# Performance work log

Hardware: AMD Instinct MI355X
Metric: run time of the kernel (lower is better)

The kernel has to match this reference:

```python
import jax, jax.numpy as jnp
import numpy as np

B, F, H, W, C = 1, 16, 32, 32, 128


def setup_inputs() -> dict:
    key = jax.random.key(0)
    ks = jax.random.split(key, 6)
    w = lambda k: jax.random.normal(k, (C, C), jnp.float32) * 0.02
    return {
        "x": jax.random.normal(ks[0], (B, F, H, W, C), jnp.float32),
        "gamma": jnp.ones((C,), jnp.float32),
        "wq": w(ks[1]), "bq": jnp.zeros((C,), jnp.float32),
        "wk": w(ks[2]), "bk": jnp.zeros((C,), jnp.float32),
        "wv": w(ks[3]), "bv": jnp.zeros((C,), jnp.float32),
        "wo": w(ks[4]), "bo": jnp.zeros((C,), jnp.float32),
    }


def reference(x, gamma, wq, bq, wk, bk, wv, bv, wo, bo):
    b, f, h, w_, c = x.shape
    s, n_hw = f * h * w_, h * w_
    identity = x

    # RMSNorm variant: L2-normalize over channels, rescale by sqrt(C) * gamma
    xn = x / (jnp.linalg.norm(x, axis=-1, keepdims=True) + 1e-8)
    xn = xn * (c ** 0.5) * gamma

    # 1x1x1 convs == pointwise linear projections; flatten to tokens [b, s, c]
    xn = xn.reshape(b, s, c)
    q = xn @ wq + bq
    k = xn @ wk + bk
    v = xn @ wv + bv

    # frame-causal block mask: query at frame i attends to all keys in frames <= i
    frame = jnp.arange(s) // n_hw                      # [s]
    allowed = frame[:, None] >= frame[None, :]          # [s, s] bool

    scale = 1.0 / jnp.sqrt(c)
    scores = jnp.einsum('bqc,bkc->bqk', q, k) * scale   # [b, s, s]
    scores = jnp.where(allowed, scores, -jnp.inf)
    attn = jax.nn.softmax(scores, axis=-1)
    out = jnp.einsum('bqk,bkc->bqc', attn, v)           # [b, s, c]

    out = out @ wo + bo
    return out.reshape(b, f, h, w_, c) + identity
```

## Files before the change

kernel.cpp:

```cpp
#include <hip/hip_runtime.h>
#include <hip/hip_bf16.h>

typedef __bf16 bf16x8 __attribute__((ext_vector_type(8)));
typedef float f32x4 __attribute__((ext_vector_type(4)));
typedef unsigned short u16;
typedef unsigned int u32;
typedef u16 ushort8 __attribute__((ext_vector_type(8)));

#define S_TOK 16384
#define C_DIM 128
#define L2E 1.4426950408889634f
#define QK_SCALE 0.08838834764831845f
#define SQRTC 11.313708498984761f

#define NBLK 512
#define TPB 34

#define WT_OFF   0u
#define BIAS_OFF 131072u
#define XN_OFF   147456u
#define O_OFF    XN_OFF
#define Q_OFF    (XN_OFF + 4194304u)
#define K_OFF    (Q_OFF + 4194304u)
#define VF_OFF   (K_OFF + 4194304u)
#define PART_OFF (VF_OFF + 4194304u)
#define ML_OFF   (PART_OFF + 20971520u)

__device__ __forceinline__ int in_is_bf16(const void* gamma) {
  return ((const u16*)gamma)[0] == 0x3F80;
}
__device__ __forceinline__ float ldf(const void* p, int i, int bf) {
  if (bf) { u32 b = ((const u16*)p)[i]; return __uint_as_float(b << 16); }
  return ((const float*)p)[i];
}
__device__ __forceinline__ float b2f(u16 b) { return __uint_as_float((u32)b << 16); }
__device__ __forceinline__ u16 f2b(float f) {
  return __builtin_bit_cast(u16, (__bf16)f);
}
__device__ __forceinline__ void gld16(const void* g, void* l) {
  __builtin_amdgcn_global_load_lds((const __attribute__((address_space(1))) u32*)g,
                                   (__attribute__((address_space(3))) u32*)l, 16, 0, 0);
}
__device__ __forceinline__ int qb_of(int t) {
  int F = 0;
  while (64 * (F + 1) * (F + 2) <= t) F++;
  int span = 16 * (F + 1);
  return 8 * F + (t - 64 * F * (F + 1)) / span;
}
__device__ __forceinline__ int start_of(int qq) {
  int Fq = qq >> 3, iq = qq & 7;
  return 16 * (Fq + 1) * (4 * Fq + iq);
}

__global__ void __launch_bounds__(256) prep_norm_kernel(const void* x, const void* gamma,
    const void* wq, const void* bq, const void* wk, const void* bk,
    const void* wv, const void* bv, const void* wo, const void* bo, char* ws) {
  int bf = in_is_bf16(gamma);
  if (blockIdx.x >= 2048) {
    int bb = blockIdx.x - 2048;
    if (bb < 256) {
      int gid = bb * 256 + threadIdx.x;
      int m = gid >> 14; int rem = gid & 16383;
      int k = rem >> 7; int n = rem & 127;
      const void* W = (m == 0) ? wq : (m == 1) ? wk : (m == 2) ? wv : wo;
      float v = ldf(W, rem, bf);
      if (m == 0) v *= QK_SCALE;
      *(u16*)(ws + WT_OFF + (u32)m * 32768u + (u32)n * 256u + (((u32)k * 2u) ^ (u32)((n & 7) << 4))) = f2b(v);
    } else {
      int idx = (bb - 256) * 256 + threadIdx.x;
      if (idx < 512) {
        int m = idx >> 7; int c = idx & 127;
        const void* B = (m == 0) ? bq : (m == 1) ? bk : (m == 2) ? bv : bo;
        float v = ldf(B, c, bf);
        if (m == 0) v *= QK_SCALE;
        ((float*)(ws + BIAS_OFF))[idx] = v;
      }
    }
    return;
  }
  int t = blockIdx.x * 256 + threadIdx.x;
  int tok = t >> 5; int sub = t & 31;
  int base = tok * 128 + sub * 4;
  float f[4];
  if (bf) {
    ushort4 v = ((const ushort4*)x)[base >> 2];
    f[0] = __uint_as_float((u32)v.x << 16); f[1] = __uint_as_float((u32)v.y << 16);
    f[2] = __uint_as_float((u32)v.z << 16); f[3] = __uint_as_float((u32)v.w << 16);
  } else {
    float4 v = ((const float4*)x)[base >> 2];
    f[0] = v.x; f[1] = v.y; f[2] = v.z; f[3] = v.w;
  }
  float ss = f[0]*f[0] + f[1]*f[1] + f[2]*f[2] + f[3]*f[3];
  #pragma unroll
  for (int m = 1; m < 32; m <<= 1) ss += __shfl_xor(ss, m);
  float fac = SQRTC / (sqrtf(ss) + 1e-8f);
  u16 o[4];
  #pragma unroll
  for (int j = 0; j < 4; j++) { float g = ldf(gamma, sub * 4 + j, bf); o[j] = f2b(f[j] * fac * g); }
  *(ushort4*)(ws + XN_OFF + (u32)tok * 256u + (((u32)sub * 8u) ^ (u32)((tok & 7) << 4))) =
      make_ushort4(o[0], o[1], o[2], o[3]);
}

__global__ void __launch_bounds__(256) qkv_kernel(char* ws) {
  __shared__ char lds[65536];
  int tid = threadIdx.x; int wid = tid >> 6; int lane = tid & 63;
  int blk = blockIdx.x & 127;
  int m = blockIdx.x >> 7;
  #pragma unroll
  for (int i = 0; i < 8; i++) {
    u32 seg = (u32)(i * 4 + wid) * 1024u;
    gld16(ws + XN_OFF + (u32)blk * 32768u + seg + (u32)lane * 16u, lds + seg);
    gld16(ws + WT_OFF + (u32)m * 32768u + seg + (u32)lane * 16u, lds + 32768 + seg);
  }
  __syncthreads();
  const float* bias = (const float*)(ws + BIAS_OFF);
  int rb = wid * 32;
  f32x4 acc[2][8];
  #pragma unroll
  for (int a = 0; a < 2; a++)
    #pragma unroll
    for (int b = 0; b < 8; b++) acc[a][b] = (f32x4){0.f, 0.f, 0.f, 0.f};
  #pragma unroll
  for (int kt = 0; kt < 4; kt++) {
    bf16x8 afr[2];
    #pragma unroll
    for (int mt = 0; mt < 2; mt++) {
      int row = rb + mt * 16 + (lane & 15);
      afr[mt] = *(const bf16x8*)(lds + row * 256 + ((kt * 64 + ((lane >> 4) * 16)) ^ ((row & 7) << 4)));
    }
    #pragma unroll
    for (int nt = 0; nt < 8; nt++) {
      int nr = nt * 16 + (lane & 15);
      bf16x8 bfr = *(const bf16x8*)(lds + 32768 + nr * 256 + ((kt * 64 + ((lane >> 4) * 16)) ^ ((nr & 7) << 4)));
      #pragma unroll
      for (int mt = 0; mt < 2; mt++)
        acc[mt][nt] = __builtin_amdgcn_mfma_f32_16x16x32_bf16(afr[mt], bfr, acc[mt][nt], 0, 0, 0);
    }
  }
  #pragma unroll
  for (int mt = 0; mt < 2; mt++)
    #pragma unroll
    for (int nt = 0; nt < 8; nt++) {
      int tok0 = blk * 128 + rb + mt * 16 + (lane >> 4) * 4;
      int c = (lane & 15) + nt * 16;
      float bv_ = bias[m * 128 + c];
      if (m == 0) {
        #pragma unroll
        for (int r = 0; r < 4; r++)
          *(u16*)(ws + Q_OFF + ((u32)(tok0 + r) * 128u + (u32)c) * 2u) = f2b(acc[mt][nt][r] + bv_);
      } else if (m == 1) {
        int ktc = c >> 5, gc = (c >> 3) & 3, jc = c & 7;
        int tile = tok0 >> 6, ntk = (tok0 >> 4) & 3, qv0 = tok0 & 15;
        char* bp = ws + K_OFF + (u32)tile * 16384u + (u32)(ktc * 4 + ntk) * 1024u + (u32)(16 * gc) * 16u + (u32)jc * 2u;
        #pragma unroll
        for (int r = 0; r < 4; r++)
          *(u16*)(bp + (u32)(qv0 + r) * 16u) = f2b(acc[mt][nt][r] + bv_);
      } else {
        int tile = tok0 >> 6, kts = (tok0 >> 5) & 1, gv = (tok0 >> 3) & 3, j0 = tok0 & 7;
        int ctv = c >> 4, qv2 = c & 15;
        u16 pk[4];
        #pragma unroll
        for (int r = 0; r < 4; r++) pk[r] = f2b(acc[mt][nt][r] + bv_);
        *(ushort4*)(ws + VF_OFF + (u32)tile * 16384u + (u32)(kts * 8 + ctv) * 1024u
                    + (u32)(qv2 + 16 * gv) * 16u + (u32)j0 * 2u) = make_ushort4(pk[0], pk[1], pk[2], pk[3]);
      }
    }
}

__global__ void __launch_bounds__(256, 2) attn_part_kernel(char* ws) {
  __shared__ char lds[65536];
  int tid = threadIdx.x; int wid = tid >> 6; int lane = tid & 63;
  int q = lane & 15; int g = lane >> 4;
  int b = blockIdx.x;
  int slot = b;
  for (int qq = 1; qq < 128; qq++) {
    int Sx = start_of(qq);
    if (Sx < TPB * b && (Sx % TPB) != 0) slot++;
  }
  char* pbase = lds + 49152 + wid * 4096;
  ushort8 ones_u;
  #pragma unroll
  for (int e = 0; e < 8; e++) ones_u[e] = 0x3F80;
  bf16x8 ones = __builtin_bit_cast(bf16x8, ones_u);

  auto stageK = [&](int t) {
    #pragma unroll
    for (int i = 0; i < 4; i++) {
      u32 off = (u32)(i * 4096) + (u32)tid * 16u;
      gld16(ws + K_OFF + (u32)t * 16384u + off, lds + off);
    }
  };
  auto stageV = [&](int t, int buf) {
    #pragma unroll
    for (int i = 0; i < 4; i++) {
      u32 off = (u32)(i * 4096) + (u32)tid * 16u;
      gld16(ws + VF_OFF + (u32)t * 16384u + off, lds + 16384 + buf * 16384 + off);
    }
  };

  int t0 = TPB * b, remaining = TPB;
  while (remaining > 0) {
    int F = 0;
    while (64 * (F + 1) * (F + 2) <= t0) F++;
    int fb = 64 * F * (F + 1); int span = 16 * (F + 1);
    int i = (t0 - fb) / span; int l = t0 - fb - i * span;
    int qb = 8 * F + i;
    int nt = min(remaining, span - l);

    bf16x8 aq0[4], aq1[4];
    {
      const char* qp0 = ws + Q_OFF + (u32)(qb * 128 + wid * 32 + q) * 256u + (u32)(g * 16);
      #pragma unroll
      for (int kt = 0; kt < 4; kt++) {
        aq0[kt] = *(const bf16x8*)(qp0 + kt * 64);
        aq1[kt] = *(const bf16x8*)(qp0 + 4096 + kt * 64);
      }
    }
    f32x4 acc0[8], acc1[8];
    #pragma unroll
    for (int z = 0; z < 8; z++) { acc0[z] = (f32x4){0.f,0.f,0.f,0.f}; acc1[z] = (f32x4){0.f,0.f,0.f,0.f}; }
    f32x4 accl0 = (f32x4){0.f,0.f,0.f,0.f}, accl1 = (f32x4){0.f,0.f,0.f,0.f};
    float m0 = -1e30f, m1 = -1e30f;
    float mL0 = m0 * L2E, mL1 = m1 * L2E;

    __syncthreads();
    stageK(l); stageV(l, 0);
    for (int it = 0; it < nt; it++) {
      int t = l + it; int cur = it & 1;
      __syncthreads();
      if (it + 1 < nt) stageV(t + 1, cur ^ 1);
      f32x4 sfr0[4], sfr1[4];
      #pragma unroll
      for (int z = 0; z < 4; z++) { sfr0[z] = (f32x4){0.f,0.f,0.f,0.f}; sfr1[z] = (f32x4){0.f,0.f,0.f,0.f}; }
      __builtin_amdgcn_s_setprio(1);
      #pragma unroll
      for (int kt = 0; kt < 4; kt++) {
        #pragma unroll
        for (int ntk = 0; ntk < 4; ntk++) {
          bf16x8 bk = *(const bf16x8*)(lds + (kt * 4 + ntk) * 1024 + (u32)lane * 16u);
          sfr0[ntk] = __builtin_amdgcn_mfma_f32_16x16x32_bf16(bk, aq0[kt], sfr0[ntk], 0, 0, 0);
          sfr1[ntk] = __builtin_amdgcn_mfma_f32_16x16x32_bf16(bk, aq1[kt], sfr1[ntk], 0, 0, 0);
        }
      }
      __builtin_amdgcn_s_setprio(0);
      float tm0 = fmaxf(fmaxf(fmaxf(sfr0[0][0], sfr0[0][1]), fmaxf(sfr0[0][2], sfr0[0][3])),
                        fmaxf(fmaxf(sfr0[1][0], sfr0[1][1]), fmaxf(sfr0[1][2], sfr0[1][3])));
      tm0 = fmaxf(tm0, fmaxf(fmaxf(fmaxf(sfr0[2][0], sfr0[2][1]), fmaxf(sfr0[2][2], sfr0[2][3])),
                             fmaxf(fmaxf(sfr0[3][0], sfr0[3][1]), fmaxf(sfr0[3][2], sfr0[3][3]))));
      float tm1 = fmaxf(fmaxf(fmaxf(sfr1[0][0], sfr1[0][1]), fmaxf(sfr1[0][2], sfr1[0][3])),
                        fmaxf(fmaxf(sfr1[1][0], sfr1[1][1]), fmaxf(sfr1[1][2], sfr1[1][3])));
      tm1 = fmaxf(tm1, fmaxf(fmaxf(fmaxf(sfr1[2][0], sfr1[2][1]), fmaxf(sfr1[2][2], sfr1[2][3])),
                             fmaxf(fmaxf(sfr1[3][0], sfr1[3][1]), fmaxf(sfr1[3][2], sfr1[3][3]))));
      tm0 = fmaxf(tm0, __shfl_xor(tm0, 16)); tm0 = fmaxf(tm0, __shfl_xor(tm0, 32));
      tm1 = fmaxf(tm1, __shfl_xor(tm1, 16)); tm1 = fmaxf(tm1, __shfl_xor(tm1, 32));
      bool need = (tm0 > m0 + 8.0f) || (tm1 > m1 + 8.0f);
      if (__any(need)) {
        float mn0 = fmaxf(m0, tm0), mn1 = fmaxf(m1, tm1);
        float a0 = exp2f((m0 - mn0) * L2E), a1 = exp2f((m1 - mn1) * L2E);
        #pragma unroll
        for (int ct = 0; ct < 8; ct++)
          #pragma unroll
          for (int r = 0; r < 4; r++) { acc0[ct][r] *= a0; acc1[ct][r] *= a1; }
        #pragma unroll
        for (int r = 0; r < 4; r++) { accl0[r] *= a0; accl1[r] *= a1; }
        m0 = mn0; m1 = mn1; mL0 = m0 * L2E; mL1 = m1 * L2E;
      }
      #pragma unroll
      for (int ntk = 0; ntk < 4; ntk++) {
        u32 dl = (u32)(q + 16 * (((ntk & 1) << 1) | (g >> 1))) * 16u + (u32)((g & 1) * 8);
        {
          float p0 = exp2f(__builtin_fmaf(sfr0[ntk][0], L2E, -mL0));
          float p1 = exp2f(__builtin_fmaf(sfr0[ntk][1], L2E, -mL0));
          float p2 = exp2f(__builtin_fmaf(sfr0[ntk][2], L2E, -mL0));
          float p3 = exp2f(__builtin_fmaf(sfr0[ntk][3], L2E, -mL0));
          u32 w0, w1;
          asm("v_cvt_pk_bf16_f32 %0, %1, %2" : "=v"(w0) : "v"(p0), "v"(p1));
          asm("v_cvt_pk_bf16_f32 %0, %1, %2" : "=v"(w1) : "v"(p2), "v"(p3));
          *(uint2*)(pbase + ((ntk >> 1) * 2 + 0) * 1024 + dl) = make_uint2(w0, w1);
        }
        {
          float p0 = exp2f(__builtin_fmaf(sfr1[ntk][0], L2E, -mL1));
          float p1 = exp2f(__builtin_fmaf(sfr1[ntk][1], L2E, -mL1));
          float p2 = exp2f(__builtin_fmaf(sfr1[ntk][2], L2E, -mL1));
          float p3 = exp2f(__builtin_fmaf(sfr1[ntk][3], L2E, -mL1));
          u32 w0, w1;
          asm("v_cvt_pk_bf16_f32 %0, %1, %2" : "=v"(w0) : "v"(p0), "v"(p1));
          asm("v_cvt_pk_bf16_f32 %0, %1, %2" : "=v"(w1) : "v"(p2), "v"(p3));
          *(uint2*)(pbase + ((ntk >> 1) * 2 + 1) * 1024 + dl) = make_uint2(w0, w1);
        }
      }
      __syncthreads();
      if (it + 1 < nt) stageK(t + 1);
      const char* vb = lds + 16384 + cur * 16384;
      __builtin_amdgcn_s_setprio(1);
      #pragma unroll
      for (int kts = 0; kts < 2; kts++) {
        bf16x8 pf0 = *(const bf16x8*)(pbase + (kts * 2 + 0) * 1024 + (u32)lane * 16u);
        bf16x8 pf1 = *(const bf16x8*)(pbase + (kts * 2 + 1) * 1024 + (u32)lane * 16u);
        accl0 = __builtin_amdgcn_mfma_f32_16x16x32_bf16(ones, pf0, accl0, 0, 0, 0);
        accl1 = __builtin_amdgcn_mfma_f32_16x16x32_bf16(ones, pf1, accl1, 0, 0, 0);
        #pragma unroll
        for (int ct = 0; ct < 8; ct++) {
          bf16x8 va = *(const bf16x8*)(vb + (kts * 8 + ct) * 1024 + (u32)lane * 16u);
          acc0[ct] = __builtin_amdgcn_mfma_f32_16x16x32_bf16(va, pf0, acc0[ct], 0, 0, 0);
          acc1[ct] = __builtin_amdgcn_mfma_f32_16x16x32_bf16(va, pf1, acc1[ct], 0, 0, 0);
        }
      }
      __builtin_amdgcn_s_setprio(0);
    }
    float l0 = accl0[0], l1 = accl1[0];
    float ri0 = 1.0f / l0, ri1 = 1.0f / l1;
    int lrow0 = wid * 32 + q;
    char* pb2 = ws + PART_OFF + (u32)slot * 32768u + (u32)lrow0 * 256u;
    #pragma unroll
    for (int ct = 0; ct < 8; ct++) {
      ushort4 pk;
      pk.x = f2b(acc0[ct][0] * ri0); pk.y = f2b(acc0[ct][1] * ri0);
      pk.z = f2b(acc0[ct][2] * ri0); pk.w = f2b(acc0[ct][3] * ri0);
      *(ushort4*)(pb2 + ct * 32 + g * 8) = pk;
      ushort4 pk1;
      pk1.x = f2b(acc1[ct][0] * ri1); pk1.y = f2b(acc1[ct][1] * ri1);
      pk1.z = f2b(acc1[ct][2] * ri1); pk1.w = f2b(acc1[ct][3] * ri1);
      *(ushort4*)(pb2 + 16 * 256 + ct * 32 + g * 8) = pk1;
    }
    if (g == 0) {
      ((float2*)(ws + ML_OFF))[slot * 128 + lrow0] = make_float2(m0, l0);
      ((float2*)(ws + ML_OFF))[slot * 128 + lrow0 + 16] = make_float2(m1, l1);
    }
    t0 += nt; remaining -= nt; slot++;
  }
}

__global__ void __launch_bounds__(256) combine_kernel(char* ws) {
  int qb = blockIdx.x >> 2;
  int seg = blockIdx.x & 3;
  int Sq = start_of(qb);
  int Eq = Sq + 16 * ((qb >> 3) + 1);
  int c_lo = Sq / TPB, c_hi = (Eq - 1) / TPB;
  int bse0 = c_lo;
  for (int qq = 1; qq < 128; qq++) {
    int Sx = start_of(qq);
    if (Sx < TPB * c_lo && (Sx % TPB) != 0) bse0++;
  }
  int tid = threadIdx.x;
  int row = seg * 32 + (tid >> 3);
  int oct = tid & 7;
  const float2* ml = (const float2*)(ws + ML_OFF);
  float M = -1e30f;
  {
    int bse = bse0;
    for (int c = c_lo; c <= c_hi; c++) {
      int qbf = qb_of(TPB * c);
      int qbl = qb_of(TPB * c + TPB - 1);
      int slot = bse + (qb - qbf);
      M = fmaxf(M, ml[slot * 128 + row].x);
      bse += qbl - qbf + 1;
    }
  }
  float a[16];
  #pragma unroll
  for (int k = 0; k < 16; k++) a[k] = 0.f;
  float D = 0.f;
  {
    int bse = bse0;
    for (int c = c_lo; c <= c_hi; c++) {
      int qbf = qb_of(TPB * c);
      int qbl = qb_of(TPB * c + TPB - 1);
      int slot = bse + (qb - qbf);
      bse += qbl - qbf + 1;
      float2 m_l = ml[slot * 128 + row];
      float w = exp2f((m_l.x - M) * L2E) * m_l.y;
      D += w;
      const u16* o = (const u16*)(ws + PART_OFF + (u32)slot * 32768u + (u32)row * 256u + (u32)oct * 32u);
      ushort8 v0 = *(const ushort8*)o;
      ushort8 v1 = *(const ushort8*)(o + 8);
      #pragma unroll
      for (int e = 0; e < 8; e++) { a[e] += w * b2f(v0[e]); a[8 + e] += w * b2f(v1[e]); }
    }
  }
  float Dinv = 1.0f / D;
  int grow = qb * 128 + row;
  ushort8 w0, w1;
  #pragma unroll
  for (int e = 0; e < 8; e++) { w0[e] = f2b(a[e] * Dinv); w1[e] = f2b(a[8 + e] * Dinv); }
  u32 rbase = (u32)grow * 256u;
  u32 swz = (u32)((row & 7) << 4);
  *(ushort8*)(ws + O_OFF + rbase + (((u32)oct * 32u) ^ swz)) = w0;
  *(ushort8*)(ws + O_OFF + rbase + (((u32)oct * 32u + 16u) ^ swz)) = w1;
}

__global__ void __launch_bounds__(256) out_kernel(const void* x, const void* gamma, char* ws, void* out) {
  __shared__ char lds[65536];
  int bf = in_is_bf16(gamma);
  int tid = threadIdx.x; int wid = tid >> 6; int lane = tid & 63;
  int blk = blockIdx.x;
  #pragma unroll
  for (int i = 0; i < 8; i++) {
    u32 seg = (u32)(i * 4 + wid) * 1024u;
    gld16(ws + O_OFF + (u32)blk * 32768u + seg + (u32)lane * 16u, lds + seg);
    gld16(ws + WT_OFF + 3u * 32768u + seg + (u32)lane * 16u, lds + 32768 + seg);
  }
  __syncthreads();
  f32x4 acc[2][8];
  #pragma unroll
  for (int a = 0; a < 2; a++)
    #pragma unroll
    for (int b = 0; b < 8; b++) acc[a][b] = (f32x4){0.f, 0.f, 0.f, 0.f};
  int rb = wid * 32;
  #pragma unroll
  for (int kt = 0; kt < 4; kt++) {
    bf16x8 afr[2];
    #pragma unroll
    for (int mt = 0; mt < 2; mt++) {
      int row = rb + mt * 16 + (lane & 15);
      afr[mt] = *(const bf16x8*)(lds + row * 256 + ((kt * 64 + ((lane >> 4) * 16)) ^ ((row & 7) << 4)));
    }
    #pragma unroll
    for (int nt = 0; nt < 8; nt++) {
      int nr = nt * 16 + (lane & 15);
      bf16x8 bfr = *(const bf16x8*)(lds + 32768 + nr * 256 + ((kt * 64 + ((lane >> 4) * 16)) ^ ((nr & 7) << 4)));
      #pragma unroll
      for (int mt = 0; mt < 2; mt++)
        acc[mt][nt] = __builtin_amdgcn_mfma_f32_16x16x32_bf16(afr[mt], bfr, acc[mt][nt], 0, 0, 0);
    }
  }
  const float* bias = (const float*)(ws + BIAS_OFF) + 3 * 128;
  #pragma unroll
  for (int mt = 0; mt < 2; mt++)
    #pragma unroll
    for (int nt = 0; nt < 8; nt++) {
      int c = (lane & 15) + nt * 16;
      float bv_ = bias[c];
      #pragma unroll
      for (int r = 0; r < 4; r++) {
        int tok = blk * 128 + rb + mt * 16 + (lane >> 4) * 4 + r;
        float v = acc[mt][nt][r] + bv_ + ldf(x, tok * 128 + c, bf);
        if (bf) ((u16*)out)[tok * 128 + c] = f2b(v);
        else    ((float*)out)[tok * 128 + c] = v;
      }
    }
}

extern "C" void kernel_launch(void* const* d_in, const int* in_sizes, int n_in,
                              void* d_out, int out_size, void* d_ws, size_t ws_size,
                              hipStream_t stream) {
  (void)in_sizes; (void)n_in; (void)out_size; (void)ws_size;
  const void* x     = d_in[0];
  const void* gamma = d_in[1];
  const void* wq = d_in[2]; const void* bq = d_in[3];
  const void* wk = d_in[4]; const void* bk = d_in[5];
  const void* wv = d_in[6]; const void* bv = d_in[7];
  const void* wo = d_in[8]; const void* bo = d_in[9];
  char* ws = (char*)d_ws;
  hipLaunchKernelGGL(prep_norm_kernel, dim3(2306), dim3(256), 0, stream,
                     x, gamma, wq, bq, wk, bk, wv, bv, wo, bo, ws);
  hipLaunchKernelGGL(qkv_kernel, dim3(384), dim3(256), 0, stream, ws);
  hipLaunchKernelGGL(attn_part_kernel, dim3(NBLK), dim3(256), 0, stream, ws);
  hipLaunchKernelGGL(combine_kernel, dim3(512), dim3(256), 0, stream, ws);
  hipLaunchKernelGGL(out_kernel, dim3(128), dim3(256), 0, stream, x, gamma, ws, d_out);
}
```

Measured before the change: 176.6 us.

## Switch attention to 32x32x16 MFMA with register-resident P via permlane32 swap

Result: no change. 175.7 us (-0.5%).

```diff
diff --git a/kernel.cpp b/kernel.cpp
--- a/kernel.cpp
+++ b/kernel.cpp
@@ -3,9 +3,11 @@
 
 typedef __bf16 bf16x8 __attribute__((ext_vector_type(8)));
 typedef float f32x4 __attribute__((ext_vector_type(4)));
+typedef float f32x16 __attribute__((ext_vector_type(16)));
 typedef unsigned short u16;
 typedef unsigned int u32;
 typedef u16 ushort8 __attribute__((ext_vector_type(8)));
+typedef u32 u32x4 __attribute__((ext_vector_type(4)));
 
 #define S_TOK 16384
 #define C_DIM 128
@@ -25,6 +27,8 @@
 #define VF_OFF   (K_OFF + 4194304u)
 #define PART_OFF (VF_OFF + 4194304u)
 #define ML_OFF   (PART_OFF + 20971520u)
+
+#define ZERO16 ((f32x16){0.f,0.f,0.f,0.f,0.f,0.f,0.f,0.f,0.f,0.f,0.f,0.f,0.f,0.f,0.f,0.f})
 
 __device__ __forceinline__ int in_is_bf16(const void* gamma) {
   return ((const u16*)gamma)[0] == 0x3F80;
@@ -149,20 +153,20 @@
         for (int r = 0; r < 4; r++)
           *(u16*)(ws + Q_OFF + ((u32)(tok0 + r) * 128u + (u32)c) * 2u) = f2b(acc[mt][nt][r] + bv_);
       } else if (m == 1) {
-        int ktc = c >> 5, gc = (c >> 3) & 3, jc = c & 7;
-        int tile = tok0 >> 6, ntk = (tok0 >> 4) & 3, qv0 = tok0 & 15;
-        char* bp = ws + K_OFF + (u32)tile * 16384u + (u32)(ktc * 4 + ntk) * 1024u + (u32)(16 * gc) * 16u + (u32)jc * 2u;
+        char* bp = ws + K_OFF + (u32)(tok0 >> 6) * 16384u
+                 + (u32)((((tok0 >> 5) & 1) << 3) + (c >> 4)) * 1024u
+                 + (u32)((tok0 & 31) + 32 * ((c >> 3) & 1)) * 16u + (u32)(c & 7) * 2u;
         #pragma unroll
         for (int r = 0; r < 4; r++)
-          *(u16*)(bp + (u32)(qv0 + r) * 16u) = f2b(acc[mt][nt][r] + bv_);
+          *(u16*)(bp + r * 16) = f2b(acc[mt][nt][r] + bv_);
       } else {
-        int tile = tok0 >> 6, kts = (tok0 >> 5) & 1, gv = (tok0 >> 3) & 3, j0 = tok0 & 7;
-        int ctv = c >> 4, qv2 = c & 15;
         u16 pk[4];
         #pragma unroll
         for (int r = 0; r < 4; r++) pk[r] = f2b(acc[mt][nt][r] + bv_);
-        *(ushort4*)(ws + VF_OFF + (u32)tile * 16384u + (u32)(kts * 8 + ctv) * 1024u
-                    + (u32)(qv2 + 16 * gv) * 16u + (u32)j0 * 2u) = make_ushort4(pk[0], pk[1], pk[2], pk[3]);
+        *(ushort4*)(ws + VF_OFF + (u32)(tok0 >> 6) * 16384u
+                    + (u32)(((c >> 5) << 2) + ((tok0 >> 4) & 3)) * 1024u
+                    + (u32)((c & 31) + 32 * ((tok0 >> 3) & 1)) * 16u + (u32)(tok0 & 7) * 2u)
+            = make_ushort4(pk[0], pk[1], pk[2], pk[3]);
       }
     }
 }
@@ -170,31 +174,30 @@
 __global__ void __launch_bounds__(256, 2) attn_part_kernel(char* ws) {
   __shared__ char lds[65536];
   int tid = threadIdx.x; int wid = tid >> 6; int lane = tid & 63;
-  int q = lane & 15; int g = lane >> 4;
+  int q = lane & 31; int hi = lane >> 5;
   int b = blockIdx.x;
   int slot = b;
   for (int qq = 1; qq < 128; qq++) {
     int Sx = start_of(qq);
     if (Sx < TPB * b && (Sx % TPB) != 0) slot++;
   }
-  char* pbase = lds + 49152 + wid * 4096;
   ushort8 ones_u;
   #pragma unroll
   for (int e = 0; e < 8; e++) ones_u[e] = 0x3F80;
   bf16x8 ones = __builtin_bit_cast(bf16x8, ones_u);
 
-  auto stageK = [&](int t) {
+  auto stageK = [&](int t, int buf) {
     #pragma unroll
     for (int i = 0; i < 4; i++) {
       u32 off = (u32)(i * 4096) + (u32)tid * 16u;
-      gld16(ws + K_OFF + (u32)t * 16384u + off, lds + off);
+      gld16(ws + K_OFF + (u32)t * 16384u + off, lds + buf * 16384 + off);
     }
   };
   auto stageV = [&](int t, int buf) {
     #pragma unroll
     for (int i = 0; i < 4; i++) {
       u32 off = (u32)(i * 4096) + (u32)tid * 16u;
-      gld16(ws + VF_OFF + (u32)t * 16384u + off, lds + 16384 + buf * 16384 + off);
+      gld16(ws + VF_OFF + (u32)t * 16384u + off, lds + 32768 + buf * 16384 + off);
     }
   };
 
@@ -207,126 +210,101 @@
     int qb = 8 * F + i;
     int nt = min(remaining, span - l);
 
-    bf16x8 aq0[4], aq1[4];
+    bf16x8 aq[8];
     {
-      const char* qp0 = ws + Q_OFF + (u32)(qb * 128 + wid * 32 + q) * 256u + (u32)(g * 16);
-      #pragma unroll
-      for (int kt = 0; kt < 4; kt++) {
-        aq0[kt] = *(const bf16x8*)(qp0 + kt * 64);
-        aq1[kt] = *(const bf16x8*)(qp0 + 4096 + kt * 64);
-      }
-    }
-    f32x4 acc0[8], acc1[8];
-    #pragma unroll
-    for (int z = 0; z < 8; z++) { acc0[z] = (f32x4){0.f,0.f,0.f,0.f}; acc1[z] = (f32x4){0.f,0.f,0.f,0.f}; }
-    f32x4 accl0 = (f32x4){0.f,0.f,0.f,0.f}, accl1 = (f32x4){0.f,0.f,0.f,0.f};
-    float m0 = -1e30f, m1 = -1e30f;
-    float mL0 = m0 * L2E, mL1 = m1 * L2E;
+      const char* qp = ws + Q_OFF + (u32)(qb * 128 + wid * 32 + q) * 256u + (u32)(hi * 16);
+      #pragma unroll
+      for (int kt = 0; kt < 8; kt++) aq[kt] = *(const bf16x8*)(qp + kt * 32);
+    }
+    f32x16 acc0 = ZERO16, acc1 = ZERO16, acc2 = ZERO16, acc3 = ZERO16, accl = ZERO16;
+    float m_run = -1e30f;
+    float mL2 = m_run * L2E;
 
     __syncthreads();
-    stageK(l); stageV(l, 0);
+    stageK(l, 0); stageV(l, 0);
     for (int it = 0; it < nt; it++) {
-      int t = l + it; int cur = it & 1;
+      int cur = it & 1;
       __syncthreads();
-      if (it + 1 < nt) stageV(t + 1, cur ^ 1);
-      f32x4 sfr0[4], sfr1[4];
-      #pragma unroll
-      for (int z = 0; z < 4; z++) { sfr0[z] = (f32x4){0.f,0.f,0.f,0.f}; sfr1[z] = (f32x4){0.f,0.f,0.f,0.f}; }
+      if (it + 1 < nt) { stageK(l + it + 1, cur ^ 1); stageV(l + it + 1, cur ^ 1); }
+      const char* kb_ = lds + cur * 16384;
+      const char* vb_ = lds + 32768 + cur * 16384;
+      f32x16 s0 = ZERO16, s1 = ZERO16;
       __builtin_amdgcn_s_setprio(1);
       #pragma unroll
-      for (int kt = 0; kt < 4; kt++) {
+      for (int kt = 0; kt < 8; kt++) {
+        bf16x8 k0 = *(const bf16x8*)(kb_ + (0 * 8 + kt) * 1024 + (u32)lane * 16u);
+        bf16x8 k1 = *(const bf16x8*)(kb_ + (1 * 8 + kt) * 1024 + (u32)lane * 16u);
+        s0 = __builtin_amdgcn_mfma_f32_32x32x16_bf16(k0, aq[kt], s0, 0, 0, 0);
+        s1 = __builtin_amdgcn_mfma_f32_32x32x16_bf16(k1, aq[kt], s1, 0, 0, 0);
+      }
+      __builtin_amdgcn_s_setprio(0);
+      float tm = s0[0];
+      #pragma unroll
+      for (int r = 1; r < 16; r++) tm = fmaxf(tm, s0[r]);
+      #pragma unroll
+      for (int r = 0; r < 16; r++) tm = fmaxf(tm, s1[r]);
+      tm = fmaxf(tm, __shfl_xor(tm, 32));
+      if (__any(tm > m_run + 8.0f)) {
+        float mnew = fmaxf(m_run, tm);
+        float alpha = exp2f((m_run - mnew) * L2E);
         #pragma unroll
-        for (int ntk = 0; ntk < 4; ntk++) {
-          bf16x8 bk = *(const bf16x8*)(lds + (kt * 4 + ntk) * 1024 + (u32)lane * 16u);
-          sfr0[ntk] = __builtin_amdgcn_mfma_f32_16x16x32_bf16(bk, aq0[kt], sfr0[ntk], 0, 0, 0);
-          sfr1[ntk] = __builtin_amdgcn_mfma_f32_16x16x32_bf16(bk, aq1[kt], sfr1[ntk], 0, 0, 0);
+        for (int r = 0; r < 16; r++) {
+          acc0[r] *= alpha; acc1[r] *= alpha; acc2[r] *= alpha; acc3[r] *= alpha; accl[r] *= alpha;
         }
+        m_run = mnew; mL2 = m_run * L2E;
+      }
+      u32 W[16];
+      #pragma unroll
+      for (int t = 0; t < 8; t++) {
+        float pa = exp2f(__builtin_fmaf(s0[2 * t], L2E, -mL2));
+        float pb = exp2f(__builtin_fmaf(s0[2 * t + 1], L2E, -mL2));
+        asm("v_cvt_pk_bf16_f32 %0, %1, %2" : "=v"(W[t]) : "v"(pa), "v"(pb));
+      }
+      #pragma unroll
+      for (int t = 0; t < 8; t++) {
+        float pa = exp2f(__builtin_fmaf(s1[2 * t], L2E, -mL2));
+        float pb = exp2f(__builtin_fmaf(s1[2 * t + 1], L2E, -mL2));
+        asm("v_cvt_pk_bf16_f32 %0, %1, %2" : "=v"(W[8 + t]) : "v"(pa), "v"(pb));
+      }
+      __builtin_amdgcn_s_setprio(1);
+      #pragma unroll
+      for (int kq = 0; kq < 4; kq++) {
+        int base = (kq >> 1) * 8 + (kq & 1) * 4;
+        u32 e0 = W[base + 0], e2 = W[base + 2];
+        u32 e1 = W[base + 1], e3 = W[base + 3];
+        asm("v_permlane32_swap_b32 %0, %1" : "+v"(e2), "+v"(e0));
+        asm("v_permlane32_swap_b32 %0, %1" : "+v"(e3), "+v"(e1));
+        u32x4 pw = (u32x4){e0, e1, e2, e3};
+        bf16x8 pfr = __builtin_bit_cast(bf16x8, pw);
+        accl = __builtin_amdgcn_mfma_f32_32x32x16_bf16(ones, pfr, accl, 0, 0, 0);
+        bf16x8 v0 = *(const bf16x8*)(vb_ + (0 * 4 + kq) * 1024 + (u32)lane * 16u);
+        bf16x8 v1 = *(const bf16x8*)(vb_ + (1 * 4 + kq) * 1024 + (u32)lane * 16u);
+        bf16x8 v2 = *(const bf16x8*)(vb_ + (2 * 4 + kq) * 1024 + (u32)lane * 16u);
+        bf16x8 v3 = *(const bf16x8*)(vb_ + (3 * 4 + kq) * 1024 + (u32)lane * 16u);
+        acc0 = __builtin_amdgcn_mfma_f32_32x32x16_bf16(v0, pfr, acc0, 0, 0, 0);
+        acc1 = __builtin_amdgcn_mfma_f32_32x32x16_bf16(v1, pfr, acc1, 0, 0, 0);
+        acc2 = __builtin_amdgcn_mfma_f32_32x32x16_bf16(v2, pfr, acc2, 0, 0, 0);
+        acc3 = __builtin_amdgcn_mfma_f32_32x32x16_bf16(v3, pfr, acc3, 0, 0, 0);
       }
       __builtin_amdgcn_s_setprio(0);
-      float tm0 = fmaxf(fmaxf(fmaxf(sfr0[0][0], sfr0[0][1]), fmaxf(sfr0[0][2], sfr0[0][3])),
-                        fmaxf(fmaxf(sfr0[1][0], sfr0[1][1]), fmaxf(sfr0[1][2], sfr0[1][3])));
-      tm0 = fmaxf(tm0, fmaxf(fmaxf(fmaxf(sfr0[2][0], sfr0[2][1]), fmaxf(sfr0[2][2], sfr0[2][3])),
-                             fmaxf(fmaxf(sfr0[3][0], sfr0[3][1]), fmaxf(sfr0[3][2], sfr0[3][3]))));
-      float tm1 = fmaxf(fmaxf(fmaxf(sfr1[0][0], sfr1[0][1]), fmaxf(sfr1[0][2], sfr1[0][3])),
-                        fmaxf(fmaxf(sfr1[1][0], sfr1[1][1]), fmaxf(sfr1[1][2], sfr1[1][3])));
-      tm1 = fmaxf(tm1, fmaxf(fmaxf(fmaxf(sfr1[2][0], sfr1[2][1]), fmaxf(sfr1[2][2], sfr1[2][3])),
-                             fmaxf(fmaxf(sfr1[3][0], sfr1[3][1]), fmaxf(sfr1[3][2], sfr1[3][3]))));
-      tm0 = fmaxf(tm0, __shfl_xor(tm0, 16)); tm0 = fmaxf(tm0, __shfl_xor(tm0, 32));
-      tm1 = fmaxf(tm1, __shfl_xor(tm1, 16)); tm1 = fmaxf(tm1, __shfl_xor(tm1, 32));
-      bool need = (tm0 > m0 + 8.0f) || (tm1 > m1 + 8.0f);
-      if (__any(need)) {
-        float mn0 = fmaxf(m0, tm0), mn1 = fmaxf(m1, tm1);
-        float a0 = exp2f((m0 - mn0) * L2E), a1 = exp2f((m1 - mn1) * L2E);
-        #pragma unroll
-        for (int ct = 0; ct < 8; ct++)
-          #pragma unroll
-          for (int r = 0; r < 4; r++) { acc0[ct][r] *= a0; acc1[ct][r] *= a1; }
-        #pragma unroll
-        for (int r = 0; r < 4; r++) { accl0[r] *= a0; accl1[r] *= a1; }
-        m0 = mn0; m1 = mn1; mL0 = m0 * L2E; mL1 = m1 * L2E;
-      }
-      #pragma unroll
-      for (int ntk = 0; ntk < 4; ntk++) {
-        u32 dl = (u32)(q + 16 * (((ntk & 1) << 1) | (g >> 1))) * 16u + (u32)((g & 1) * 8);
-        {
-          float p0 = exp2f(__builtin_fmaf(sfr0[ntk][0], L2E, -mL0));
-          float p1 = exp2f(__builtin_fmaf(sfr0[ntk][1], L2E, -mL0));
-          float p2 = exp2f(__builtin_fmaf(sfr0[ntk][2], L2E, -mL0));
-          float p3 = exp2f(__builtin_fmaf(sfr0[ntk][3], L2E, -mL0));
-          u32 w0, w1;
-          asm("v_cvt_pk_bf16_f32 %0, %1, %2" : "=v"(w0) : "v"(p0), "v"(p1));
-          asm("v_cvt_pk_bf16_f32 %0, %1, %2" : "=v"(w1) : "v"(p2), "v"(p3));
-          *(uint2*)(pbase + ((ntk >> 1) * 2 + 0) * 1024 + dl) = make_uint2(w0, w1);
-        }
-        {
-          float p0 = exp2f(__builtin_fmaf(sfr1[ntk][0], L2E, -mL1));
-          float p1 = exp2f(__builtin_fmaf(sfr1[ntk][1], L2E, -mL1));
-          float p2 = exp2f(__builtin_fmaf(sfr1[ntk][2], L2E, -mL1));
-          float p3 = exp2f(__builtin_fmaf(sfr1[ntk][3], L2E, -mL1));
-          u32 w0, w1;
-          asm("v_cvt_pk_bf16_f32 %0, %1, %2" : "=v"(w0) : "v"(p0), "v"(p1));
-          asm("v_cvt_pk_bf16_f32 %0, %1, %2" : "=v"(w1) : "v"(p2), "v"(p3));
-          *(uint2*)(pbase + ((ntk >> 1) * 2 + 1) * 1024 + dl) = make_uint2(w0, w1);
-        }
-      }
-      __syncthreads();
-      if (it + 1 < nt) stageK(t + 1);
-      const char* vb = lds + 16384 + cur * 16384;
-      __builtin_amdgcn_s_setprio(1);
-      #pragma unroll
-      for (int kts = 0; kts < 2; kts++) {
-        bf16x8 pf0 = *(const bf16x8*)(pbase + (kts * 2 + 0) * 1024 + (u32)lane * 16u);
-        bf16x8 pf1 = *(const bf16x8*)(pbase + (kts * 2 + 1) * 1024 + (u32)lane * 16u);
-        accl0 = __builtin_amdgcn_mfma_f32_16x16x32_bf16(ones, pf0, accl0, 0, 0, 0);
-        accl1 = __builtin_amdgcn_mfma_f32_16x16x32_bf16(ones, pf1, accl1, 0, 0, 0);
-        #pragma unroll
-        for (int ct = 0; ct < 8; ct++) {
-          bf16x8 va = *(const bf16x8*)(vb + (kts * 8 + ct) * 1024 + (u32)lane * 16u);
-          acc0[ct] = __builtin_amdgcn_mfma_f32_16x16x32_bf16(va, pf0, acc0[ct], 0, 0, 0);
-          acc1[ct] = __builtin_amdgcn_mfma_f32_16x16x32_bf16(va, pf1, acc1[ct], 0, 0, 0);
-        }
-      }
-      __builtin_amdgcn_s_setprio(0);
-    }
-    float l0 = accl0[0], l1 = accl1[0];
-    float ri0 = 1.0f / l0, ri1 = 1.0f / l1;
-    int lrow0 = wid * 32 + q;
-    char* pb2 = ws + PART_OFF + (u32)slot * 32768u + (u32)lrow0 * 256u;
-    #pragma unroll
-    for (int ct = 0; ct < 8; ct++) {
-      ushort4 pk;
-      pk.x = f2b(acc0[ct][0] * ri0); pk.y = f2b(acc0[ct][1] * ri0);
-      pk.z = f2b(acc0[ct][2] * ri0); pk.w = f2b(acc0[ct][3] * ri0);
-      *(ushort4*)(pb2 + ct * 32 + g * 8) = pk;
-      ushort4 pk1;
-      pk1.x = f2b(acc1[ct][0] * ri1); pk1.y = f2b(acc1[ct][1] * ri1);
-      pk1.z = f2b(acc1[ct][2] * ri1); pk1.w = f2b(acc1[ct][3] * ri1);
-      *(ushort4*)(pb2 + 16 * 256 + ct * 32 + g * 8) = pk1;
-    }
-    if (g == 0) {
-      ((float2*)(ws + ML_OFF))[slot * 128 + lrow0] = make_float2(m0, l0);
-      ((float2*)(ws + ML_OFF))[slot * 128 + lrow0 + 16] = make_float2(m1, l1);
-    }
+    }
+    float l_run = accl[0];
+    float rinv = 1.0f / l_run;
+    int lrow = wid * 32 + q;
+    char* pb2 = ws + PART_OFF + (u32)slot * 32768u + (u32)lrow * 256u;
+    #pragma unroll
+    for (int cb = 0; cb < 4; cb++) {
+      const f32x16* A = (cb == 0) ? &acc0 : (cb == 1) ? &acc1 : (cb == 2) ? &acc2 : &acc3;
+      #pragma unroll
+      for (int t = 0; t < 8; t++) {
+        float fa = (*A)[2 * t] * rinv, fb = (*A)[2 * t + 1] * rinv;
+        u32 w;
+        asm("v_cvt_pk_bf16_f32 %0, %1, %2" : "=v"(w) : "v"(fa), "v"(fb));
+        int ch = cb * 32 + 8 * (t >> 1) + 2 * (t & 1) + 4 * hi;
+        *(u32*)(pb2 + ch * 2) = w;
+      }
+    }
+    if (hi == 0) ((float2*)(ws + ML_OFF))[slot * 128 + lrow] = make_float2(m_run, l_run);
     t0 += nt; remaining -= nt; slot++;
   }
 }
```
